# Kernel tuning notes

Hardware: AMD Instinct MI355X
Metric: run time of the kernel (lower is better)

Reference implementation:

```python
import jax, jax.numpy as jnp
import numpy as np

B, T_ENC, T_DEC = 1024, 96, 16
P_Q, CFG, H = 235, 32, 256
D_IN = P_Q + 5 + 10 + 3 + 3  # 256, matches input_size in __init__


def _lstm_step(x, h, c, Wih, Whh, bih, bhh):
    # torch.nn.LSTMCell: gate order i, f, g, o
    g = x @ Wih.T + bih + h @ Whh.T + bhh
    i, f, gg, o = jnp.split(g, 4, axis=-1)
    c2 = jax.nn.sigmoid(f) * c + jax.nn.sigmoid(i) * jnp.tanh(gg)
    h2 = jax.nn.sigmoid(o) * jnp.tanh(c2)
    return h2, c2


def setup_inputs():
    key = jax.random.key(0)
    ks = jax.random.split(key, 30)
    s = 0.05

    def n(i, shape):
        return jax.random.normal(ks[i], shape, jnp.float32) * s

    return {
        "input_p_q": jax.random.normal(ks[0], (B, T_ENC, P_Q), jnp.float32),
        "input_config": jax.random.normal(ks[1], (B, T_ENC, CFG), jnp.float32),
        "input_time": jax.random.randint(ks[2], (B, T_ENC, 3), 0, 5, jnp.int32),
        "W_cfg": n(3, (10, CFG)), "b_cfg": n(4, (10,)),
        "E_hour": n(5, (24, 5)), "E_wd": n(6, (8, 3)), "E_season": n(7, (5, 3)),
        "Wih_e": n(8, (4 * H, D_IN)), "Whh_e": n(9, (4 * H, H)),
        "bih_e": n(10, (4 * H,)), "bhh_e": n(11, (4 * H,)),
        "Wih_d": n(12, (4, H + 1)), "Whh_d": n(13, (4, 1)),
        "bih_d": n(14, (4,)), "bhh_d": n(15, (4,)),
        "Wi_s": n(16, (H, D_IN)), "bi_s": n(17, (H,)),
        "We_s": n(18, (H, 2 * H)),
        "Vd_s": n(19, (1, H)), "bVd_s": n(20, (1,)),
        "Wd_t": n(21, (H, H)), "bd_t": n(22, (H,)),
        "Wd2_t": n(23, (H, 2)),
        "Vd_t": n(24, (1, H)), "bVd_t": n(25, (1,)),
    }


def _forward(input_p_q, input_config, input_time, W_cfg, b_cfg, E_hour, E_wd, E_season,
             Wih_e, Whh_e, bih_e, bhh_e, Wih_d, Whh_d, bih_d, bhh_d,
             Wi_s, bi_s, We_s, Vd_s, bVd_s, Wd_t, bd_t, Wd2_t, Vd_t, bVd_t):
    b = input_p_q.shape[0]
    cfg = input_config @ W_cfg.T + b_cfg  # [B,T,10]
    inputs = jnp.concatenate([
        input_p_q, cfg,
        E_hour[input_time[:, :, 0]],
        E_wd[input_time[:, :, 1]],
        E_season[input_time[:, :, 2]],
    ], axis=2)  # [B,T,D_IN]

    # spatial_attention_Wi(inputs) hoisted out of the per-step loop (identical math)
    wi = inputs @ Wi_s.T + bi_s  # [B,T,H]

    def enc_step(carry, xt):
        hi, ci = carry
        x_t, wi_t = xt
        # Vd(tanh(We([h,c]) + Wi(x)))  -> [B,1] scalar gate (no softmax in original)
        a = jnp.tanh(jnp.concatenate([hi, ci], axis=1) @ We_s.T + wi_t) @ Vd_s.T + bVd_s
        h2, c2 = _lstm_step(x_t * a, hi, ci, Wih_e, Whh_e, bih_e, bhh_e)
        return (h2, c2), h2

    h0 = jnp.zeros((b, H), inputs.dtype)
    (_, _), mid = jax.lax.scan(enc_step, (h0, h0),
                               (inputs.transpose(1, 0, 2), wi.transpose(1, 0, 2)))
    mid = mid.transpose(1, 0, 2)  # [B,T,H]

    # temporal_attention_Wd(mid) does not depend on decode step -> hoisted
    wd_mid = mid @ Wd_t.T + bd_t  # [B,T,H]
    prev0 = mid[:, -1, 2:3]       # [B,1], as in original (element 2 of last hidden)

    def dec_step(carry, _):
        hi, ci, prev = carry
        q = jnp.concatenate([hi, ci], axis=1) @ Wd2_t.T       # [B,H]
        a = jnp.tanh(q[:, None, :] + wd_mid) @ Vd_t.T + bVd_t  # [B,T,1], raw scores
        ctx = jnp.einsum('bth,bt->bh', mid, a[..., 0])          # weighted sum over T
        h2, c2 = _lstm_step(jnp.concatenate([ctx, prev], axis=1), hi, ci,
                            Wih_d, Whh_d, bih_d, bhh_d)
        return (h2, c2, h2), h2

    z = jnp.zeros((b, 1), inputs.dtype)
    _, dec = jax.lax.scan(dec_step, (z, z, prev0), None, length=T_DEC)
    return dec.transpose(1, 0, 2)  # [B,16,1]


def reference(input_p_q, input_config, input_time, W_cfg, b_cfg, E_hour, E_wd, E_season,
              Wih_e, Whh_e, bih_e, bhh_e, Wih_d, Whh_d, bih_d, bhh_d,
              Wi_s, bi_s, We_s, Vd_s, bVd_s, Wd_t, bd_t, Wd2_t, Vd_t, bVd_t):
    return _forward(input_p_q, input_config, input_time, W_cfg, b_cfg, E_hour, E_wd,
                    E_season, Wih_e, Whh_e, bih_e, bhh_e, Wih_d, Whh_d, bih_d, bhh_d,
                    Wi_s, bi_s, We_s, Vd_s, bVd_s, Wd_t, bd_t, Wd2_t, Vd_t, bVd_t)
```

## Files before the change

kernel.cpp:

```cpp
#include <hip/hip_runtime.h>
#include <hip/hip_bf16.h>


typedef unsigned short ushort_t;
using short4v = __attribute__((ext_vector_type(4))) short;
using short8  = __attribute__((ext_vector_type(8))) short;
using floatx4 = __attribute__((ext_vector_type(4))) float;

#define DEVFN static __device__ __forceinline__

DEVFN float bs2f(ushort_t u) {
    union { float f; unsigned v; } c; c.v = ((unsigned)u) << 16; return c.f;
}
DEVFN ushort_t f2bs(float f) {
    __hip_bfloat16 h = __float2bfloat16(f);
    return *reinterpret_cast<ushort_t*>(&h);
}
DEVFN float gload(const void* p, long i, int bf) {
    if (bf) return bs2f(((const ushort_t*)p)[i]);
    return ((const float*)p)[i];
}
DEVFN float sigm(float x) { return 1.f / (1.f + __expf(-x)); }
DEVFN float ftanh(float x) {
    float t = __expf(-2.f * fabsf(x));
    float r = (1.f - t) / (1.f + t);
    return copysignf(r, x);
}
DEVFN short8 ld8(const ushort_t* p) { return *reinterpret_cast<const short8*>(p); }

DEVFN void bar_lgkm() {
    asm volatile("s_waitcnt lgkmcnt(0)" ::: "memory");
    __builtin_amdgcn_s_barrier();
}

#define GLD16R(dst, src) \
    asm volatile("global_load_dwordx4 %0, %1, off" : "+v"(dst) : "v"(src))

#define VW3() do { asm volatile("s_waitcnt vmcnt(3)"); \
                   __builtin_amdgcn_sched_barrier(0x3F7); } while (0)

struct SrcPtrs { const void* p[26]; };
struct WsPtrs {
    ushort_t *wcfg, *bcfg, *eh, *ew, *es, *wis, *bis, *wes, *vds, *bvds,
             *whh, *wih, *bih, *bhh, *wdt, *bdt, *wd2t, *vdt, *bvdt,
             *wihd, *whhd, *bihd, *bhhd;
};

__global__ void k_detect(const void* probe, int* flag) {
    if (threadIdx.x == 0 && blockIdx.x == 0) {
        const ushort_t* u = (const ushort_t*)probe;
        int ok = 1;
        for (int i = 0; i < 16; ++i) {
            ushort_t v = u[2 * i];
            int e = (v >> 7) & 0xFF;
            if (!(v == 0 || (e >= 96 && e <= 126))) ok = 0;
        }
        *flag = ok;
    }
}

__global__ __launch_bounds__(256) void k_cvt(SrcPtrs sp, WsPtrs wp, const int* flagp) {
    int bf = *flagp;
    const void* src = nullptr; ushort_t* dst = nullptr; long n = 0;
    switch (blockIdx.x) {
        case 0:  src = sp.p[3];  dst = wp.wcfg; n = 320;    break;
        case 1:  src = sp.p[4];  dst = wp.bcfg; n = 10;     break;
        case 2:  src = sp.p[5];  dst = wp.eh;   n = 120;    break;
        case 3:  src = sp.p[6];  dst = wp.ew;   n = 24;     break;
        case 4:  src = sp.p[7];  dst = wp.es;   n = 15;     break;
        case 5:  src = sp.p[16]; dst = wp.wis;  n = 65536;  break;
        case 6:  src = sp.p[17]; dst = wp.bis;  n = 256;    break;
        case 8:  src = sp.p[19]; dst = wp.vds;  n = 256;    break;
        case 9:  src = sp.p[20]; dst = wp.bvds; n = 1;      break;
        case 12: src = sp.p[10]; dst = wp.bih;  n = 1024;   break;
        case 13: src = sp.p[11]; dst = wp.bhh;  n = 1024;   break;
        case 14: src = sp.p[21]; dst = wp.wdt;  n = 65536;  break;
        case 15: src = sp.p[22]; dst = wp.bdt;  n = 256;    break;
        case 16: src = sp.p[23]; dst = wp.wd2t; n = 512;    break;
        case 17: src = sp.p[24]; dst = wp.vdt;  n = 256;    break;
        case 18: src = sp.p[25]; dst = wp.bvdt; n = 1;      break;
        case 19: src = sp.p[12]; dst = wp.wihd; n = 1028;   break;
        case 20: src = sp.p[13]; dst = wp.whhd; n = 4;      break;
        case 21: src = sp.p[14]; dst = wp.bihd; n = 4;      break;
        case 22: src = sp.p[15]; dst = wp.bhhd; n = 4;      break;
        default: return;
    }
    for (long i = threadIdx.x; i < n; i += 256) {
        float v = bf ? bs2f(((const ushort_t*)src)[i]) : ((const float*)src)[i];
        dst[i] = f2bs(v);
    }
}

__global__ __launch_bounds__(256) void k_permA(
    const void* whh_src, const void* wih_src,
    ushort_t* whhp, ushort_t* wihb, const int* flagp)
{
    int bf = *flagp;
    long base = (long)blockIdx.x * 2048;
    if (blockIdx.y == 1) {
#pragma unroll
        for (int ii = 0; ii < 8; ++ii) {
            long p = base + threadIdx.x + ii * 256;
            wihb[p] = f2bs(gload(wih_src, p, bf));
        }
        return;
    }
#pragma unroll
    for (int ii = 0; ii < 8; ++ii) {
        long p = base + threadIdx.x + ii * 256;
        int c = (int)(p >> 9), l = (int)((p >> 3) & 63), e = (int)(p & 7);
        int w = c >> 5, kk = (c >> 2) & 7, g = c & 3;
        int q = l >> 4, ln = l & 15;
        long si = (long)(g * 256 + w * 16 + ln) * 256 + kk * 32 + q * 8 + e;
        whhp[p] = f2bs(gload(whh_src, si, bf));
    }
}

__global__ __launch_bounds__(256) void k_permB(
    const void* wes_src, ushort_t* wesp, const int* flagp)
{
    int bf = *flagp;
    long base = (long)blockIdx.x * 2048;
#pragma unroll
    for (int ii = 0; ii < 8; ++ii) {
        long p = base + threadIdx.x + ii * 256;
        int c = (int)(p >> 9), l = (int)((p >> 3) & 63), e = (int)(p & 7);
        int w = c >> 4, kk = c & 15;
        int q = l >> 4, ln = l & 15;
        long si = (long)(w * 16 + ln) * 512 + kk * 32 + q * 8 + e;
        wesp[p] = f2bs(gload(wes_src, si, bf));
    }
}

__global__ __launch_bounds__(256) void k_build(
    const void* __restrict__ pq, const void* __restrict__ cfg_in,
    const int* __restrict__ timei, WsPtrs wp, const int* __restrict__ flagp,
    ushort_t* __restrict__ inputs)
{
    int bf = *flagp;
    int ch = threadIdx.x;
    for (int rr = 0; rr < 4; ++rr) {
        long row = (long)blockIdx.x * 4 + rr;
        float v;
        if (ch < 235) {
            v = gload(pq, row * 235 + ch, bf);
        } else if (ch < 245) {
            int j = ch - 235;
            float acc = bs2f(wp.bcfg[j]);
            for (int k = 0; k < 32; ++k)
                acc += gload(cfg_in, row * 32 + k, bf) * bs2f(wp.wcfg[j * 32 + k]);
            v = acc;
        } else if (ch < 250) {
            v = bs2f(wp.eh[timei[row * 3 + 0] * 5 + (ch - 245)]);
        } else if (ch < 253) {
            v = bs2f(wp.ew[timei[row * 3 + 1] * 3 + (ch - 250)]);
        } else {
            v = bs2f(wp.es[timei[row * 3 + 2] * 3 + (ch - 253)]);
        }
        inputs[row * 256 + ch] = f2bs(v);
    }
}

#define MFMA16(a, b, c) __builtin_amdgcn_mfma_f32_16x16x32_bf16((a), (b), (c), 0, 0, 0)

__global__ __launch_bounds__(256) void k_gemmN(
    const ushort_t* __restrict__ A, const ushort_t* __restrict__ Wg,
    const ushort_t* __restrict__ Ws, const ushort_t* __restrict__ bias,
    ushort_t* __restrict__ outg, ushort_t* __restrict__ outs,
    int nax, int ns)
{
    __shared__ alignas(16) ushort_t At[128][264];
    __shared__ alignas(16) ushort_t Bt[128][40];

    int tid  = threadIdx.x;
    int lane = tid & 63, wave = tid >> 6;
    int wm = wave >> 1, wn = wave & 1;
    int q = lane >> 4, ln = lane & 15;
    long mbase = (long)blockIdx.x * 128;

#pragma unroll
    for (int it = 0; it < 16; ++it) {
        int idx = tid + it * 256;
        int r = idx >> 5, u = idx & 31;
        *reinterpret_cast<short8*>(&At[r][u * 8]) =
            ld8(&A[(mbase + r) * 256 + u * 8]);
    }
    __syncthreads();

    const int ny = nax + ns;
    for (int y = 0; y < ny; ++y) {
        floatx4 acc[4][4];
#pragma unroll
        for (int i = 0; i < 4; ++i)
#pragma unroll
            for (int j = 0; j < 4; ++j) acc[i][j] = (floatx4){0.f, 0.f, 0.f, 0.f};

        for (int k0 = 0; k0 < 256; k0 += 32) {
            __syncthreads();
#pragma unroll
            for (int it = 0; it < 2; ++it) {
                int c = tid + it * 256;
                int r = c >> 2, kc = (c & 3) * 8;
                const ushort_t* src;
                if (y < nax) {
                    int wrow = ((r & 3) << 8) + (y << 5) + (r >> 2);
                    src = &Wg[(long)wrow * 256 + k0 + kc];
                } else {
                    int wrow = ((y - nax) << 7) + r;
                    src = &Ws[(long)wrow * 256 + k0 + kc];
                }
                *reinterpret_cast<short8*>(&Bt[r][kc]) = ld8(src);
            }
            __syncthreads();
            short8 af[4];
#pragma unroll
            for (int mt = 0; mt < 4; ++mt)
                af[mt] = ld8(&At[wm * 64 + mt * 16 + ln][k0 + q * 8]);
#pragma unroll
            for (int nt = 0; nt < 4; ++nt) {
                short8 bf = ld8(&Bt[wn * 64 + nt * 16 + ln][q * 8]);
#pragma unroll
                for (int mt = 0; mt < 4; ++mt)
                    acc[mt][nt] = MFMA16(af[mt], bf, acc[mt][nt]);
            }
        }

#pragma unroll
        for (int mt = 0; mt < 4; ++mt)
#pragma unroll
            for (int nt = 0; nt < 4; ++nt)
#pragma unroll
                for (int reg = 0; reg < 4; ++reg) {
                    long row = mbase + wm * 64 + mt * 16 + q * 4 + reg;
                    int  cc  = wn * 64 + nt * 16 + ln;
                    if (y < nax) {
                        int col = (y << 7) + cc;
                        outg[row * 1024L + col] = f2bs(acc[mt][nt][reg]);
                    } else {
                        int col = ((y - nax) << 7) + cc;
                        outs[row * 256L + col] =
                            f2bs(acc[mt][nt][reg] + bs2f(bias[col]));
                    }
                }
    }
}

__global__ __launch_bounds__(512) void k_encoder(
    const ushort_t* __restrict__ wi, const ushort_t* __restrict__ ax,
    WsPtrs wp, ushort_t* __restrict__ mid)
{
    __shared__ alignas(16) ushort_t hcb[2][16][520];
    __shared__ alignas(16) float aPartT[16][20];
    __shared__ ushort_t occupancy_pad[30720];

    int tid  = threadIdx.x;
    int lane = tid & 63, w = tid >> 6;
    int q = lane >> 4, ln = lane & 15;
    long row0 = (long)blockIdx.x * 16;
    int u0 = w * 32 + ln;

    for (int i = tid; i < 2 * 16 * 520; i += 512) ((ushort_t*)hcb)[i] = 0;

    float bc[2][4], vds[2];
#pragma unroll
    for (int s = 0; s < 2; ++s) {
        int us = u0 + s * 16;
        bc[s][0] = bs2f(wp.bih[us])       + bs2f(wp.bhh[us]);
        bc[s][1] = bs2f(wp.bih[256 + us]) + bs2f(wp.bhh[256 + us]);
        bc[s][2] = bs2f(wp.bih[512 + us]) + bs2f(wp.bhh[512 + us]);
        bc[s][3] = bs2f(wp.bih[768 + us]) + bs2f(wp.bhh[768 + us]);
        vds[s]   = bs2f(wp.vds[us]);
    }
    float bVd = bs2f(wp.bvds[0]);

    const ushort_t* wesW0 = wp.wes + ((long)(2 * w)     << 13) + lane * 8;
    const ushort_t* wesW1 = wp.wes + ((long)(2 * w + 1) << 13) + lane * 8;
    const ushort_t* whhW0 = wp.whh + ((long)(2 * w)     << 14) + lane * 8;
    const ushort_t* whhW1 = wp.whh + ((long)(2 * w + 1) << 14) + lane * 8;

    const ushort_t* wiB0 = wi + ((row0 + q * 4) * 96) * 256 + u0;
    const ushort_t* axB0 = ax + ((row0 + q * 4) * 96) * 1024 + u0 * 4;

    int mr = tid >> 5, mc = (tid & 31) * 8;
    ushort_t* midB = mid + (row0 + mr) * 96 * 256 + mc;

    if (blockIdx.x > 60000) {
        occupancy_pad[tid] = (ushort_t)tid;
        midB[0] = occupancy_pad[(tid + 1) & 511];
    }

    float creg[2][4] = {{0.f, 0.f, 0.f, 0.f}, {0.f, 0.f, 0.f, 0.f}};
    __syncthreads();

    auto sp3 = [&](int j) -> const ushort_t* {
        if (j < 16)  return wesW0 + ((j & 15) << 9);
        if (j < 32)  return wesW1 + ((j & 15) << 9);
        if (j < 64)  return whhW0 + (((j - 32) & 31) << 9);
        return whhW1 + (((j - 64) & 31) << 9);
    };

    short8 Wr[4] = {};
#pragma unroll
    for (int j = 0; j < 4; ++j) GLD16R(Wr[j], sp3(j));

    for (int t = 0; t < 96; ++t) {
        ushort_t (*R)[520]  = hcb[t & 1];
        ushort_t (*Wb)[520] = hcb[(t & 1) ^ 1];

        {
            long toff = (long)(t > 0 ? t - 1 : 95) * 256;
            uint4 hv = *reinterpret_cast<const uint4*>(&R[mr][mc]);
            *reinterpret_cast<uint4*>(midB + toff) = hv;
        }
        short4v axv[2][4]; float wiv[2][4];
#pragma unroll
        for (int reg = 0; reg < 4; ++reg) {
            const ushort_t* a0 = axB0 + ((long)reg * 96 + t) * 1024;
            axv[0][reg] = *reinterpret_cast<const short4v*>(a0);
            axv[1][reg] = *reinterpret_cast<const short4v*>(a0 + 64);
            const ushort_t* w0 = wiB0 + ((long)reg * 96 + t) * 256;
            wiv[0][reg] = bs2f(w0[0]);
            wiv[1][reg] = bs2f(w0[16]);
        }

#pragma unroll
        for (int s = 0; s < 2; ++s) {
            floatx4 acc1 = (floatx4){0.f, 0.f, 0.f, 0.f};
#pragma unroll
            for (int c = 0; c < 16; ++c) {
                const int j = s * 16 + c;
                short8 af = ld8(&R[ln][c * 32 + q * 8]);
                VW3();
                acc1 = MFMA16(af, Wr[j & 3], acc1);
                GLD16R(Wr[j & 3], sp3((j + 4) % 96));
            }
            float p4[4];
#pragma unroll
            for (int reg = 0; reg < 4; ++reg)
                p4[reg] = ftanh(acc1[reg] + wiv[s][reg]) * vds[s];
#pragma unroll
            for (int m = 1; m < 16; m <<= 1) {
#pragma unroll
                for (int reg = 0; reg < 4; ++reg)
                    p4[reg] += __shfl_xor(p4[reg], m, 64);
            }
            if (ln == 0) {
                floatx4 pv = {p4[0], p4[1], p4[2], p4[3]};
                *reinterpret_cast<floatx4*>(&aPartT[2 * w + s][q * 4]) = pv;
            }
        }
        bar_lgkm();

        floatx4 av = {bVd, bVd, bVd, bVd};
#pragma unroll
        for (int ww = 0; ww < 16; ++ww)
            av += *reinterpret_cast<const floatx4*>(&aPartT[ww][q * 4]);

#pragma unroll
        for (int s = 0; s < 2; ++s) {
            floatx4 aH[4];
#pragma unroll
            for (int g = 0; g < 4; ++g) aH[g] = (floatx4){0.f, 0.f, 0.f, 0.f};
#pragma unroll
            for (int kk = 0; kk < 8; ++kk) {
                short8 af = ld8(&R[ln][kk * 32 + q * 8]);
#pragma unroll
                for (int g = 0; g < 4; ++g) {
                    const int j = 32 + s * 32 + kk * 4 + g;
                    VW3();
                    aH[g] = MFMA16(af, Wr[j & 3], aH[g]);
                    GLD16R(Wr[j & 3], sp3((j + 4) % 96));
                }
            }
            int us = u0 + s * 16;
#pragma unroll
            for (int reg = 0; reg < 4; ++reg) {
                float a  = av[reg];
                float gi = aH[0][reg] + a * bs2f((ushort_t)axv[s][reg][0]) + bc[s][0];
                float gf = aH[1][reg] + a * bs2f((ushort_t)axv[s][reg][1]) + bc[s][1];
                float gg = aH[2][reg] + a * bs2f((ushort_t)axv[s][reg][2]) + bc[s][2];
                float go = aH[3][reg] + a * bs2f((ushort_t)axv[s][reg][3]) + bc[s][3];
                float c2 = sigm(gf) * creg[s][reg] + sigm(gi) * ftanh(gg);
                float h2 = sigm(go) * ftanh(c2);
                creg[s][reg] = c2;
                int r = q * 4 + reg;
                Wb[r][us] = f2bs(h2);
                Wb[r][256 + us] = f2bs(c2);
            }
        }
        bar_lgkm();
    }

    asm volatile("s_waitcnt vmcnt(0)" ::: "memory");
    {
        uint4 hv = *reinterpret_cast<const uint4*>(&hcb[0][mr][mc]);
        *reinterpret_cast<uint4*>(midB + 95L * 256) = hv;
    }
}

__global__ __launch_bounds__(256) void k_decoder(
    const ushort_t* __restrict__ mid, const ushort_t* __restrict__ wd,
    WsPtrs wp, const int* __restrict__ flagp, void* __restrict__ out)
{
    __shared__ ushort_t wdl[96][264];
    __shared__ float qL[256], aLs[96], ctxL[256], VdtL[256], gL[4];
    __shared__ float st[3];

    int tid = threadIdx.x;
    long b = blockIdx.x;
    int bf = *flagp;

    for (int c = tid; c < 96 * 256; c += 256) {
        int tp = c >> 8, chn = c & 255;
        wdl[tp][chn] = wd[(b * 96 + tp) * 256 + chn];
    }
    qL[tid] = 0.f; ctxL[tid] = 0.f;
    if (tid < 96) aLs[tid] = 0.f;
    if (tid < 4)  gL[tid] = 0.f;
    VdtL[tid] = bs2f(wp.vdt[tid]);
    if (tid == 0) {
        st[0] = 0.f; st[1] = 0.f;
        st[2] = bs2f(mid[(b * 96 + 95) * 256 + 2]);
    }
    float bVdt = bs2f(wp.bvdt[0]);
    float w2a = bs2f(wp.wd2t[tid * 2]), w2b = bs2f(wp.wd2t[tid * 2 + 1]);
    __syncthreads();

    for (int s = 0; s < 16; ++s) {
        float hi = st[0], ci = st[1], prev = st[2];
        qL[tid] = hi * w2a + ci * w2b;
        __syncthreads();
        {
            int v = tid >> 6, l = tid & 63;
            for (int tp = v; tp < 96; tp += 4) {
                float sacc = 0.f;
#pragma unroll
                for (int e = 0; e < 4; ++e) {
                    int u = l * 4 + e;
                    sacc += ftanh(qL[u] + bs2f(wdl[tp][u])) * VdtL[u];
                }
#pragma unroll
                for (int m = 1; m < 64; m <<= 1) sacc += __shfl_xor(sacc, m, 64);
                if (l == 0) aLs[tp] = sacc + bVdt;
            }
        }
        __syncthreads();
        {
            float acc = 0.f;
            for (int tp = 0; tp < 96; ++tp)
                acc += aLs[tp] * bs2f(mid[(b * 96 + tp) * 256 + tid]);
            ctxL[tid] = acc;
        }
        __syncthreads();
        {
            int g = tid >> 6, k = tid & 63;
            float part = 0.f;
#pragma unroll
            for (int e = 0; e < 4; ++e) {
                int u = k + e * 64;
                part += bs2f(wp.wihd[g * 257 + u]) * ctxL[u];
            }
#pragma unroll
            for (int m = 1; m < 64; m <<= 1) part += __shfl_xor(part, m, 64);
            if (k == 0)
                gL[g] = part + bs2f(wp.bihd[g]) + bs2f(wp.bhhd[g])
                      + bs2f(wp.whhd[g]) * hi + bs2f(wp.wihd[g * 257 + 256]) * prev;
        }
        __syncthreads();
        if (tid == 0) {
            float c2 = sigm(gL[1]) * ci + sigm(gL[0]) * ftanh(gL[2]);
            float h2 = sigm(gL[3]) * ftanh(c2);
            st[0] = h2; st[1] = c2; st[2] = h2;
            long oi = b * 16 + s;
            if (bf) ((ushort_t*)out)[oi] = f2bs(h2);
            else    ((float*)out)[oi] = h2;
        }
        __syncthreads();
    }
}

extern "C" void kernel_launch(void* const* d_in, const int* in_sizes, int n_in,
                              void* d_out, int out_size, void* d_ws, size_t ws_size,
                              hipStream_t stream)
{
    const long MT = 1024L * 96;

    int* flagp = (int*)d_ws;
    ushort_t* base = (ushort_t*)((char*)d_ws + 256);

    SrcPtrs sp;
    for (int i = 0; i < 26; ++i) sp.p[i] = d_in[i];

    static const long sizes[23] = {
        320, 10, 120, 24, 15, 65536, 256, 131072, 256, 1,
        262144, 262144, 1024, 1024, 65536, 256, 512, 256, 1,
        1028, 4, 4, 4
    };
    ushort_t* ptrs[23];
    long off = 0;
    for (int i = 0; i < 23; ++i) {
        ptrs[i] = base + off;
        off += (sizes[i] + 7) & ~7L;
    }

    WsPtrs wp;
    wp.wcfg = ptrs[0];  wp.bcfg = ptrs[1];  wp.eh   = ptrs[2];  wp.ew   = ptrs[3];
    wp.es   = ptrs[4];  wp.wis  = ptrs[5];  wp.bis  = ptrs[6];  wp.wes  = ptrs[7];
    wp.vds  = ptrs[8];  wp.bvds = ptrs[9];  wp.whh  = ptrs[10]; wp.wih  = ptrs[11];
    wp.bih  = ptrs[12]; wp.bhh  = ptrs[13]; wp.wdt  = ptrs[14]; wp.bdt  = ptrs[15];
    wp.wd2t = ptrs[16]; wp.vdt  = ptrs[17]; wp.bvdt = ptrs[18]; wp.wihd = ptrs[19];
    wp.whhd = ptrs[20]; wp.bihd = ptrs[21]; wp.bhhd = ptrs[22];

    ushort_t* inputs = base + off;
    ushort_t* wib    = inputs + MT * 256;
    ushort_t* midb   = wib + MT * 256;
    ushort_t* axb    = midb + MT * 256;
    ushort_t* wdb    = wib;

    k_detect<<<1, 64, 0, stream>>>(d_in[3], flagp);
    k_cvt<<<23, 256, 0, stream>>>(sp, wp, flagp);
    k_permA<<<dim3(128, 2), 256, 0, stream>>>(d_in[9], d_in[8], wp.whh, wp.wih, flagp);
    k_permB<<<64, 256, 0, stream>>>(d_in[18], wp.wes, flagp);
    k_build<<<24576, 256, 0, stream>>>(d_in[0], d_in[1], (const int*)d_in[2],
                                       wp, flagp, inputs);
    k_gemmN<<<768, 256, 0, stream>>>(inputs, wp.wih, wp.wis, wp.bis,
                                     axb, wib, 8, 2);
    k_encoder<<<64, 512, 0, stream>>>(wib, axb, wp, midb);
    k_gemmN<<<768, 256, 0, stream>>>(midb, nullptr, wp.wdt, wp.bdt,
                                     nullptr, wdb, 0, 2);
    k_decoder<<<1024, 256, 0, stream>>>(midb, wdb, wp, flagp, d_out);
}
```

Measured before the change: 2.306 ms.

## Cache part of We_s in LDS for encoder and merge weight-prep kernels

The encoder now stages the first 12 of 96 per-step weight chunks (We_s for the first slot) in shared memory once, instead of streaming them from global/L2 every timestep, and renumbers the remaining register-prefetch ring to 84 chunks. The dummy shared-memory occupancy padding is replaced by this real cache, keeping LDS usage similar. The three weight conversion/permutation kernels are merged into one launch to cut launch overhead. The change relies on LDS reads being cheaper than the global prefetch path, and it alters the prefetch schedule.

```diff
diff --git a/kernel.cpp b/kernel.cpp
--- a/kernel.cpp
+++ b/kernel.cpp
@@ -59,76 +59,74 @@
     }
 }
 
-__global__ __launch_bounds__(256) void k_cvt(SrcPtrs sp, WsPtrs wp, const int* flagp) {
+__global__ __launch_bounds__(256) void k_prep(SrcPtrs sp, WsPtrs wp, const int* flagp) {
     int bf = *flagp;
-    const void* src = nullptr; ushort_t* dst = nullptr; long n = 0;
-    switch (blockIdx.x) {
-        case 0:  src = sp.p[3];  dst = wp.wcfg; n = 320;    break;
-        case 1:  src = sp.p[4];  dst = wp.bcfg; n = 10;     break;
-        case 2:  src = sp.p[5];  dst = wp.eh;   n = 120;    break;
-        case 3:  src = sp.p[6];  dst = wp.ew;   n = 24;     break;
-        case 4:  src = sp.p[7];  dst = wp.es;   n = 15;     break;
-        case 5:  src = sp.p[16]; dst = wp.wis;  n = 65536;  break;
-        case 6:  src = sp.p[17]; dst = wp.bis;  n = 256;    break;
-        case 8:  src = sp.p[19]; dst = wp.vds;  n = 256;    break;
-        case 9:  src = sp.p[20]; dst = wp.bvds; n = 1;      break;
-        case 12: src = sp.p[10]; dst = wp.bih;  n = 1024;   break;
-        case 13: src = sp.p[11]; dst = wp.bhh;  n = 1024;   break;
-        case 14: src = sp.p[21]; dst = wp.wdt;  n = 65536;  break;
-        case 15: src = sp.p[22]; dst = wp.bdt;  n = 256;    break;
-        case 16: src = sp.p[23]; dst = wp.wd2t; n = 512;    break;
-        case 17: src = sp.p[24]; dst = wp.vdt;  n = 256;    break;
-        case 18: src = sp.p[25]; dst = wp.bvdt; n = 1;      break;
-        case 19: src = sp.p[12]; dst = wp.wihd; n = 1028;   break;
-        case 20: src = sp.p[13]; dst = wp.whhd; n = 4;      break;
-        case 21: src = sp.p[14]; dst = wp.bihd; n = 4;      break;
-        case 22: src = sp.p[15]; dst = wp.bhhd; n = 4;      break;
-        default: return;
-    }
-    for (long i = threadIdx.x; i < n; i += 256) {
-        float v = bf ? bs2f(((const ushort_t*)src)[i]) : ((const float*)src)[i];
-        dst[i] = f2bs(v);
-    }
-}
-
-__global__ __launch_bounds__(256) void k_permA(
-    const void* whh_src, const void* wih_src,
-    ushort_t* whhp, ushort_t* wihb, const int* flagp)
-{
-    int bf = *flagp;
-    long base = (long)blockIdx.x * 2048;
-    if (blockIdx.y == 1) {
+    int b = (int)blockIdx.x;
+
+    if (b < 23) {
+        const void* src = nullptr; ushort_t* dst = nullptr; long n = 0;
+        switch (b) {
+            case 0:  src = sp.p[3];  dst = wp.wcfg; n = 320;    break;
+            case 1:  src = sp.p[4];  dst = wp.bcfg; n = 10;     break;
+            case 2:  src = sp.p[5];  dst = wp.eh;   n = 120;    break;
+            case 3:  src = sp.p[6];  dst = wp.ew;   n = 24;     break;
+            case 4:  src = sp.p[7];  dst = wp.es;   n = 15;     break;
+            case 5:  src = sp.p[16]; dst = wp.wis;  n = 65536;  break;
+            case 6:  src = sp.p[17]; dst = wp.bis;  n = 256;    break;
+            case 8:  src = sp.p[19]; dst = wp.vds;  n = 256;    break;
+            case 9:  src = sp.p[20]; dst = wp.bvds; n = 1;      break;
+            case 12: src = sp.p[10]; dst = wp.bih;  n = 1024;   break;
+            case 13: src = sp.p[11]; dst = wp.bhh;  n = 1024;   break;
+            case 14: src = sp.p[21]; dst = wp.wdt;  n = 65536;  break;
+            case 15: src = sp.p[22]; dst = wp.bdt;  n = 256;    break;
+            case 16: src = sp.p[23]; dst = wp.wd2t; n = 512;    break;
+            case 17: src = sp.p[24]; dst = wp.vdt;  n = 256;    break;
+            case 18: src = sp.p[25]; dst = wp.bvdt; n = 1;      break;
+            case 19: src = sp.p[12]; dst = wp.wihd; n = 1028;   break;
+            case 20: src = sp.p[13]; dst = wp.whhd; n = 4;      break;
+            case 21: src = sp.p[14]; dst = wp.bihd; n = 4;      break;
+            case 22: src = sp.p[15]; dst = wp.bhhd; n = 4;      break;
+            default: return;
+        }
+        for (long i = threadIdx.x; i < n; i += 256) {
+            float v = bf ? bs2f(((const ushort_t*)src)[i]) : ((const float*)src)[i];
+            dst[i] = f2bs(v);
+        }
+        return;
+    }
+    if (b < 151) {
+        long base = (long)(b - 23) * 2048;
 #pragma unroll
         for (int ii = 0; ii < 8; ++ii) {
             long p = base + threadIdx.x + ii * 256;
-            wihb[p] = f2bs(gload(wih_src, p, bf));
+            int c = (int)(p >> 9), l = (int)((p >> 3) & 63), e = (int)(p & 7);
+            int w = c >> 5, kk = (c >> 2) & 7, g = c & 3;
+            int q = l >> 4, ln = l & 15;
+            long si = (long)(g * 256 + w * 16 + ln) * 256 + kk * 32 + q * 8 + e;
+            wp.whh[p] = f2bs(gload(sp.p[9], si, bf));
         }
         return;
     }
-#pragma unroll
-    for (int ii = 0; ii < 8; ++ii) {
-        long p = base + threadIdx.x + ii * 256;
-        int c = (int)(p >> 9), l = (int)((p >> 3) & 63), e = (int)(p & 7);
-        int w = c >> 5, kk = (c >> 2) & 7, g = c & 3;
-        int q = l >> 4, ln = l & 15;
-        long si = (long)(g * 256 + w * 16 + ln) * 256 + kk * 32 + q * 8 + e;
-        whhp[p] = f2bs(gload(whh_src, si, bf));
-    }
-}
-
-__global__ __launch_bounds__(256) void k_permB(
-    const void* wes_src, ushort_t* wesp, const int* flagp)
-{
-    int bf = *flagp;
-    long base = (long)blockIdx.x * 2048;
-#pragma unroll
-    for (int ii = 0; ii < 8; ++ii) {
-        long p = base + threadIdx.x + ii * 256;
-        int c = (int)(p >> 9), l = (int)((p >> 3) & 63), e = (int)(p & 7);
-        int w = c >> 4, kk = c & 15;
-        int q = l >> 4, ln = l & 15;
-        long si = (long)(w * 16 + ln) * 512 + kk * 32 + q * 8 + e;
-        wesp[p] = f2bs(gload(wes_src, si, bf));
+    if (b < 279) {
+        long base = (long)(b - 151) * 2048;
+#pragma unroll
+        for (int ii = 0; ii < 8; ++ii) {
+            long p = base + threadIdx.x + ii * 256;
+            wp.wih[p] = f2bs(gload(sp.p[8], p, bf));
+        }
+        return;
+    }
+    {
+        long base = (long)(b - 279) * 2048;
+#pragma unroll
+        for (int ii = 0; ii < 8; ++ii) {
+            long p = base + threadIdx.x + ii * 256;
+            int c = (int)(p >> 9), l = (int)((p >> 3) & 63), e = (int)(p & 7);
+            int w = c >> 4, kk = c & 15;
+            int q = l >> 4, ln = l & 15;
+            long si = (long)(w * 16 + ln) * 512 + kk * 32 + q * 8 + e;
+            wp.wes[p] = f2bs(gload(sp.p[18], si, bf));
+        }
     }
 }
 
@@ -249,9 +247,9 @@
     const ushort_t* __restrict__ wi, const ushort_t* __restrict__ ax,
     WsPtrs wp, ushort_t* __restrict__ mid)
 {
+    __shared__ ushort_t wcache[8][12][512];
     __shared__ alignas(16) ushort_t hcb[2][16][520];
     __shared__ alignas(16) float aPartT[16][20];
-    __shared__ ushort_t occupancy_pad[30720];
 
     int tid  = threadIdx.x;
     int lane = tid & 63, w = tid >> 6;
@@ -284,24 +282,23 @@
     int mr = tid >> 5, mc = (tid & 31) * 8;
     ushort_t* midB = mid + (row0 + mr) * 96 * 256 + mc;
 
-    if (blockIdx.x > 60000) {
-        occupancy_pad[tid] = (ushort_t)tid;
-        midB[0] = occupancy_pad[(tid + 1) & 511];
-    }
+#pragma unroll
+    for (int c = 0; c < 12; ++c)
+        *reinterpret_cast<short8*>(&wcache[w][c][lane * 8]) = ld8(wesW0 + (c << 9));
 
     float creg[2][4] = {{0.f, 0.f, 0.f, 0.f}, {0.f, 0.f, 0.f, 0.f}};
     __syncthreads();
 
-    auto sp3 = [&](int j) -> const ushort_t* {
-        if (j < 16)  return wesW0 + ((j & 15) << 9);
-        if (j < 32)  return wesW1 + ((j & 15) << 9);
-        if (j < 64)  return whhW0 + (((j - 32) & 31) << 9);
-        return whhW1 + (((j - 64) & 31) << 9);
+    auto sp3m = [&](int m) -> const ushort_t* {
+        if (m < 4)   return wesW0 + ((m + 12) << 9);
+        if (m < 20)  return wesW1 + ((m - 4) << 9);
+        if (m < 52)  return whhW0 + ((m - 20) << 9);
+        return whhW1 + ((m - 52) << 9);
     };
 
     short8 Wr[4] = {};
 #pragma unroll
-    for (int j = 0; j < 4; ++j) GLD16R(Wr[j], sp3(j));
+    for (int m = 0; m < 4; ++m) GLD16R(Wr[m], sp3m(m));
 
     for (int t = 0; t < 96; ++t) {
         ushort_t (*R)[520]  = hcb[t & 1];
@@ -328,11 +325,16 @@
             floatx4 acc1 = (floatx4){0.f, 0.f, 0.f, 0.f};
 #pragma unroll
             for (int c = 0; c < 16; ++c) {
-                const int j = s * 16 + c;
                 short8 af = ld8(&R[ln][c * 32 + q * 8]);
-                VW3();
-                acc1 = MFMA16(af, Wr[j & 3], acc1);
-                GLD16R(Wr[j & 3], sp3((j + 4) % 96));
+                if (s == 0 && c < 12) {
+                    short8 bw = ld8(&wcache[w][c][lane * 8]);
+                    acc1 = MFMA16(af, bw, acc1);
+                } else {
+                    const int m = (s == 0) ? (c - 12) : (c + 4);
+                    VW3();
+                    acc1 = MFMA16(af, Wr[m & 3], acc1);
+                    GLD16R(Wr[m & 3], sp3m((m + 4) % 84));
+                }
             }
             float p4[4];
 #pragma unroll
@@ -366,10 +368,10 @@
                 short8 af = ld8(&R[ln][kk * 32 + q * 8]);
 #pragma unroll
                 for (int g = 0; g < 4; ++g) {
-                    const int j = 32 + s * 32 + kk * 4 + g;
+                    const int m = 20 + s * 32 + kk * 4 + g;
                     VW3();
-                    aH[g] = MFMA16(af, Wr[j & 3], aH[g]);
-                    GLD16R(Wr[j & 3], sp3((j + 4) % 96));
+                    aH[g] = MFMA16(af, Wr[m & 3], aH[g]);
+                    GLD16R(Wr[m & 3], sp3m((m + 4) % 84));
                 }
             }
             int us = u0 + s * 16;
@@ -518,9 +520,7 @@
     ushort_t* wdb    = wib;
 
     k_detect<<<1, 64, 0, stream>>>(d_in[3], flagp);
-    k_cvt<<<23, 256, 0, stream>>>(sp, wp, flagp);
-    k_permA<<<dim3(128, 2), 256, 0, stream>>>(d_in[9], d_in[8], wp.whh, wp.wih, flagp);
-    k_permB<<<64, 256, 0, stream>>>(d_in[18], wp.wes, flagp);
+    k_prep<<<343, 256, 0, stream>>>(sp, wp, flagp);
     k_build<<<24576, 256, 0, stream>>>(d_in[0], d_in[1], (const int*)d_in[2],
                                        wp, flagp, inputs);
     k_gemmN<<<768, 256, 0, stream>>>(inputs, wp.wih, wp.wis, wp.bis,
```

Result: faster. 2.117 ms (-8.2%).
